# Kernel optimization log

Hardware: AMD Instinct MI355X
Metric: run time of the kernel (lower is better)

The kernel has to match this reference:

```python
import jax, jax.numpy as jnp
import numpy as np
from functools import partial

V, H, B, T, L = 32000, 1024, 64, 64, 4
EOS = 2


def setup_inputs() -> dict:
    key = jax.random.key(0)
    ks = jax.random.split(key, 10)
    s = 1.0 / np.sqrt(H)
    return {
        "max_len": T,
        "tgt": jax.random.randint(ks[0], (B, T), 0, V),
        "h0": jax.random.normal(ks[1], (L, B, H), jnp.float32),
        "c0": jax.random.normal(ks[2], (L, B, H), jnp.float32),
        "embedding": jax.random.normal(ks[3], (V, H), jnp.float32) * s,
        "W_ih": jax.random.normal(ks[4], (L, 4 * H, H), jnp.float32) * s,
        "W_hh": jax.random.normal(ks[5], (L, 4 * H, H), jnp.float32) * s,
        "b_ih": jax.random.normal(ks[6], (L, 4 * H), jnp.float32) * s,
        "b_hh": jax.random.normal(ks[7], (L, 4 * H), jnp.float32) * s,
        "W_cls": jax.random.normal(ks[8], (V, H), jnp.float32) * s,
        "b_cls": jax.random.normal(ks[9], (V,), jnp.float32) * s,
    }


def _lstm_cell(x, h, c, Wi, Wh, bi, bh):
    # gates: [B, 4H] in torch order (i, f, g, o)
    g = x @ Wi.T + bi + h @ Wh.T + bh
    i, f, gg, o = jnp.split(g, 4, axis=-1)
    c2 = jax.nn.sigmoid(f) * c + jax.nn.sigmoid(i) * jnp.tanh(gg)
    h2 = jax.nn.sigmoid(o) * jnp.tanh(c2)
    return h2, c2


def reference(max_len, tgt, h0, c0, embedding, W_ih, W_hh, b_ih, b_hh, W_cls, b_cls):
    # step i>0 uses embedding of tgt[:, i-1].
    batch = tgt.shape[0]
    x0 = jnp.broadcast_to(embedding[EOS], (batch, embedding.shape[1]))
    tf_in = embedding[tgt[:, : max_len - 1]]              # [B, T-1, H]
    inputs = jnp.concatenate([x0[:, None, :], tf_in], axis=1)  # [B, T, H]
    inputs = jnp.swapaxes(inputs, 0, 1)                   # [T, B, H]

    def step(carry, x):
        h, c = carry  # each [L, B, H]
        hs, cs = [], []
        inp = x
        for l in range(L):  # 4 stacked LSTM cells, h of cell l feeds cell l+1
            hn, cn = _lstm_cell(inp, h[l], c[l], W_ih[l], W_hh[l], b_ih[l], b_hh[l])
            hs.append(hn)
            cs.append(cn)
            inp = hn
        h = jnp.stack(hs)
        c = jnp.stack(cs)
        logp = jax.nn.log_softmax(h[L - 1] @ W_cls.T + b_cls, axis=-1)  # [B, V]
        return (h, c), logp

    (h, c), out = jax.lax.scan(step, (h0, c0), inputs)
    return out, h, c  # out: [T, B, V]
```

## Files before the change

### kernel.cpp

```cpp
#include <hip/hip_runtime.h>

using u16 = unsigned short;
using u32 = unsigned int;

typedef __bf16 bf16x8 __attribute__((ext_vector_type(8)));
typedef float  f32x4  __attribute__((ext_vector_type(4)));
typedef u16    u16x8  __attribute__((ext_vector_type(8)));

static constexpr int kV = 32000, kH = 1024, kB = 64, kT = 64, kL = 4, kEOS = 2;

struct Flag { int v; int pad[15]; };

__device__ __forceinline__ u16 f2bf(float f) {
  u32 u = __float_as_uint(f);
  u = (u + 0x7fffu + ((u >> 16) & 1u)) >> 16;
  return (u16)u;
}
__device__ __forceinline__ float sigf(float x)   { return 1.0f / (1.0f + __expf(-x)); }
__device__ __forceinline__ float tanhf_(float x) { return 1.0f - 2.0f / (__expf(2.0f * x) + 1.0f); }

typedef const __attribute__((address_space(1))) u32* gas_ptr;
typedef __attribute__((address_space(3))) u32*       las_ptr;
__device__ __forceinline__ void async16(const u16* g, u16* l) {
  __builtin_amdgcn_global_load_lds((gas_ptr)g, (las_ptr)l, 16, 0, 0);
}

__device__ __forceinline__ void spin_ge(const int* p, int tgt) {
  while (__hip_atomic_load(p, __ATOMIC_RELAXED, __HIP_MEMORY_SCOPE_AGENT) < tgt)
    __builtin_amdgcn_s_sleep(2);
}

__device__ __forceinline__ size_t packed_off(int b, int k) {
  return (size_t)(((b >> 4) * 32 + (k >> 5)) * 512 + (((k >> 3) & 3) * 16 + (b & 15)) * 8 + (k & 7));
}


__global__ void pack_lstm(const float* __restrict__ Wih, const float* __restrict__ Whh,
                          u16* __restrict__ wpack) {
  const int cid  = blockIdx.x * 256 + threadIdx.x;
  const int lane = cid & 63;
  const int cf   = (cid >> 6) & 3;
  const int kk   = (cid >> 8) & 31;
  const int mt   = (cid >> 13) & 1;
  const int blk  = cid >> 14;
  const int lay = blk >> 6, cb = blk & 63;
  const int wr = cf * 1024 + cb * 16 + (lane & 15);
  const int kb = kk * 32 + (lane >> 4) * 8;
  const float* src = (mt ? Whh : Wih) + ((size_t)lay * 4096 + wr) * 1024 + kb;
  const float4* s4 = (const float4*)src;
  float4 v0 = s4[0], v1 = s4[1];
  u16x8 r;
  r[0]=f2bf(v0.x); r[1]=f2bf(v0.y); r[2]=f2bf(v0.z); r[3]=f2bf(v0.w);
  r[4]=f2bf(v1.x); r[5]=f2bf(v1.y); r[6]=f2bf(v1.z); r[7]=f2bf(v1.w);
  *(u16x8*)(wpack + (size_t)cid * 8) = r;
}

__global__ void pack_cls(const float* __restrict__ W, u16* __restrict__ o) {
  const size_t cid = (size_t)blockIdx.x * 256 + threadIdx.x;
  const float4* s4 = (const float4*)(W + cid * 8);
  float4 v0 = s4[0], v1 = s4[1];
  u16x8 r;
  r[0]=f2bf(v0.x); r[1]=f2bf(v0.y); r[2]=f2bf(v0.z); r[3]=f2bf(v0.w);
  r[4]=f2bf(v1.x); r[5]=f2bf(v1.y); r[6]=f2bf(v1.z); r[7]=f2bf(v1.w);
  *(u16x8*)(o + cid * 8) = r;
}

__global__ void pack_x(const float* __restrict__ emb, const int* __restrict__ tgt,
                       u16* __restrict__ X) {
  const int cid = blockIdx.x * 256 + threadIdx.x;
  const int kc = cid & 127, b = (cid >> 7) & 63, t = cid >> 13;
  const int tok = (t == 0) ? kEOS : tgt[b * 64 + t - 1];
  const float4* s4 = (const float4*)(emb + (size_t)tok * 1024 + kc * 8);
  float4 v0 = s4[0], v1 = s4[1];
  u16x8 r;
  r[0]=f2bf(v0.x); r[1]=f2bf(v0.y); r[2]=f2bf(v0.z); r[3]=f2bf(v0.w);
  r[4]=f2bf(v1.x); r[5]=f2bf(v1.y); r[6]=f2bf(v1.z); r[7]=f2bf(v1.w);
  *(u16x8*)(X + (size_t)t * 65536 + packed_off(b, kc * 8)) = r;
}

__global__ void pack_init(const float* __restrict__ h0, const float* __restrict__ bih,
                          const float* __restrict__ bhh, u16* __restrict__ hball,
                          float* __restrict__ bsum) {
  const int cid = blockIdx.x * 256 + threadIdx.x;
  if (cid < 32768) {
    const int kc = cid & 127, row = cid >> 7;
    const int lay = row >> 6, b = row & 63;
    const float4* s4 = (const float4*)(h0 + (size_t)cid * 8);
    float4 v0 = s4[0], v1 = s4[1];
    u16x8 r;
    r[0]=f2bf(v0.x); r[1]=f2bf(v0.y); r[2]=f2bf(v0.z); r[3]=f2bf(v0.w);
    r[4]=f2bf(v1.x); r[5]=f2bf(v1.y); r[6]=f2bf(v1.z); r[7]=f2bf(v1.w);
    *(u16x8*)(hball + (size_t)lay * 65 * 65536 + packed_off(b, kc * 8)) = r;
  } else {
    const int i = cid - 32768;
    bsum[i] = bih[i] + bhh[i];
  }
}

__global__ void __launch_bounds__(1024, 4)
lstm_coop(const u16* __restrict__ wpack, const u16* __restrict__ xall,
          u16* __restrict__ hball, const float* __restrict__ bsum,
          const float* __restrict__ c0, float* __restrict__ outh, float* __restrict__ outc,
          Flag* flags) {
  __shared__ u16 stg[3][32][512];
  __shared__ float Gc[2][64][80];

  const int tid = threadIdx.x, lane = tid & 63, wave = tid >> 6;
  const int l15 = lane & 15, l4 = lane >> 4;
  const int cmat = wave >> 3, cwc = (wave >> 1) & 3, ckh = wave & 1;
  const int blk = blockIdx.x;
  const int lay = (blk >> 1) & 3;
  const int cb  = ((blk >> 3) << 1) | (blk & 1);
  const int u0 = cb << 4;
  const int ub = tid >> 4, uu = tid & 15;

  float creg = c0[((size_t)lay * 64 + ub) * 1024 + u0 + uu];
  float bsv[4];
  #pragma unroll
  for (int g = 0; g < 4; ++g) bsv[g] = bsum[lay * 4096 + g * 1024 + u0 + uu];

  const size_t wbase = (size_t)(lay * 64 + cb) * 131072;
  bf16x8 breg[16];
  #pragma unroll
  for (int j = 0; j < 16; ++j)
    breg[j] = *(const bf16x8*)(wpack + wbase
        + (size_t)(((cmat * 32 + 2 * j + ckh) * 4) + cwc) * 512 + lane * 8);

  const int j0 = wave * 2, j1 = wave * 2 + 1;
  const int m2a = j0 >> 4, mta = (j0 >> 2) & 3, ksla = j0 & 3;
  const int m2b = j1 >> 4, mtb = (j1 >> 2) & 3, kslb = j1 & 3;

  u16* hlay = hball + (size_t)lay * 65 * 65536;
  const u16* hprev = (lay == 0) ? xall : (hball + (size_t)(lay - 1) * 65 * 65536);

  #pragma unroll 1
  for (int t = 0; t < kT; ++t) {
    if (t > 0 && tid < 64)                 spin_ge(&flags[lay * 64 + tid].v, t);
    if (lay > 0 && tid >= 64 && tid < 128) spin_ge(&flags[(lay - 1) * 64 + (tid - 64)].v, t + 1);
    __syncthreads();

    const u16* xsrc = (lay == 0) ? (xall + (size_t)t * 65536)
                                 : (hprev + (size_t)(t + 1) * 65536);
    const u16* hsrc = hlay + (size_t)t * 65536;

    const u16* ga = (m2a ? hsrc : xsrc) + (size_t)((mta * 32 + ksla) * 512) + lane * 8;
    const u16* gb = (m2b ? hsrc : xsrc) + (size_t)((mtb * 32 + kslb) * 512) + lane * 8;

    auto STAGE = [&](int c) {
      async16(ga + (size_t)c * 2048, &stg[c % 3][m2a * 16 + mta * 4 + ksla][0]);
      async16(gb + (size_t)c * 2048, &stg[c % 3][m2b * 16 + mtb * 4 + kslb][0]);
    };

    f32x4 acc[4] = {};
    STAGE(0); STAGE(1);
    #pragma unroll
    for (int c = 0; c < 8; ++c) {
      if (c < 7) asm volatile("s_waitcnt vmcnt(2)" ::: "memory");
      else       asm volatile("s_waitcnt vmcnt(0)" ::: "memory");
      __builtin_amdgcn_s_barrier();
      asm volatile("" ::: "memory");
      if (c < 6) STAGE(c + 2);
      const u16* As = &stg[c % 3][cmat * 16][0];
      #pragma unroll
      for (int s = 0; s < 2; ++s) {
        const int ksl = 2 * s + ckh;
        bf16x8 a[4];
        #pragma unroll
        for (int m = 0; m < 4; ++m)
          a[m] = *(const bf16x8*)(As + (m * 4 + ksl) * 512 + lane * 8);
        #pragma unroll
        for (int m = 0; m < 4; ++m)
          acc[m] = __builtin_amdgcn_mfma_f32_16x16x32_bf16(a[m], breg[2 * c + s], acc[m], 0, 0, 0);
      }
    }

    if (ckh == 0) {
      #pragma unroll
      for (int m = 0; m < 4; ++m)
        #pragma unroll
        for (int r = 0; r < 4; ++r)
          Gc[cmat][m * 16 + l4 * 4 + r][cwc * 16 + l15] = acc[m][r];
    }
    __syncthreads();
    if (ckh == 1) {
      #pragma unroll
      for (int m = 0; m < 4; ++m)
        #pragma unroll
        for (int r = 0; r < 4; ++r)
          Gc[cmat][m * 16 + l4 * 4 + r][cwc * 16 + l15] += acc[m][r];
    }
    __syncthreads();

    float sg[4];
    #pragma unroll
    for (int g = 0; g < 4; ++g) {
      const int col = g * 16 + uu;
      sg[g] = Gc[0][ub][col] + Gc[1][ub][col] + bsv[g];
    }
    const float c2 = sigf(sg[1]) * creg + sigf(sg[0]) * tanhf_(sg[2]);
    const float h2 = sigf(sg[3]) * tanhf_(c2);
    creg = c2;
    const u16 hv = f2bf(h2);
    if (t == kT - 1) {
      outh[((size_t)lay * 64 + ub) * 1024 + u0 + uu] = h2;
      outc[((size_t)lay * 64 + ub) * 1024 + u0 + uu] = c2;
    }
    const u32 other = __shfl_xor((u32)hv, 1);
    if ((tid & 1) == 0) {
      const u32 hpair = (u32)hv | (other << 16);
      u32* hdst = (u32*)(hlay + (size_t)(t + 1) * 65536 + packed_off(ub, u0 + uu));
      __hip_atomic_store(hdst, hpair, __ATOMIC_RELAXED, __HIP_MEMORY_SCOPE_AGENT);
    }
    __syncthreads();
    if (tid == 0)
      __hip_atomic_store(&flags[lay * 64 + cb].v, t + 1, __ATOMIC_RELAXED, __HIP_MEMORY_SCOPE_AGENT);
  }
}

#define CLS_EPILOGUE()                                                                     \
  {                                                                                        \
    float* sR = (float*)&sA[0][0];                                                         \
    _Pragma("unroll")                                                                      \
    for (int mi = 0; mi < 4; ++mi) {                                                       \
      _Pragma("unroll")                                                                    \
      for (int r = 0; r < 4; ++r) {                                                        \
        float v[4];                                                                        \
        _Pragma("unroll")                                                                  \
        for (int ci = 0; ci < 4; ++ci) v[ci] = acc[mi][ci][r] + bc[ci];                     \
        float mx = fmaxf(fmaxf(v[0], v[1]), fmaxf(v[2], v[3]));                            \
        mx = fmaxf(mx, __shfl_xor(mx, 1)); mx = fmaxf(mx, __shfl_xor(mx, 2));              \
        mx = fmaxf(mx, __shfl_xor(mx, 4)); mx = fmaxf(mx, __shfl_xor(mx, 8));              \
        float ss = __expf(v[0]-mx) + __expf(v[1]-mx) + __expf(v[2]-mx) + __expf(v[3]-mx);  \
        ss += __shfl_xor(ss, 1); ss += __shfl_xor(ss, 2);                                  \
        ss += __shfl_xor(ss, 4); ss += __shfl_xor(ss, 8);                                  \
        const int lr = wm * 64 + mi * 16 + l4 * 4 + r;                                     \
        if (wc == 0 && l15 == 0) { sR[lr * 2] = mx; sR[lr * 2 + 1] = ss; }                 \
        __syncthreads();                                                                   \
        if (wc == 1 && l15 == 0) {                                                         \
          const float m0 = sR[lr * 2], s0 = sR[lr * 2 + 1];                                \
          const float M = fmaxf(m0, mx);                                                   \
          const float S = s0 * __expf(m0 - M) + ss * __expf(mx - M);                       \
          const int grow = bm * 128 + lr;                                                  \
          pmax[(size_t)grow * 256 + bn] = M;                                               \
          psum[(size_t)grow * 256 + bn] = S;                                               \
        }                                                                                  \
        __syncthreads();                                                                   \
      }                                                                                    \
    }                                                                                      \
  }

__global__ void __launch_bounds__(256)
cls_gemm(const u16* __restrict__ A, const u16* __restrict__ Bw,
         const float* __restrict__ bcls, float* __restrict__ out,
         float* __restrict__ pmax, float* __restrict__ psum) {
  __shared__ u16 sA[2][4096], sB[2][4096];
  const int tid = threadIdx.x, lane = tid & 63, wave = tid >> 6;
  const int wm = wave >> 1, wc = wave & 1;
  const int l15 = lane & 15, l4 = lane >> 4;
  const int bm = blockIdx.x, bn = blockIdx.y;
  const u16* Ab = A  + (size_t)bm * 131072;
  const u16* Bb = Bw + (size_t)bn * 131072;

  auto STAGE = [&](int kk) {
    u16* dA = sA[kk & 1]; u16* dB = sB[kk & 1];
    #pragma unroll
    for (int q = 0; q < 4; ++q) {
      const int u = wave * 4 + q;
      if (u < 8) {
        const u16* g = Ab + (size_t)(u >> 2) * 65536 + (size_t)(((u & 3) * 32 + kk) * 512) + lane * 8;
        async16(g, dA + u * 512);
      } else {
        const int v = u & 7;
        const u16* g = Bb + (size_t)((v & 1) * 64 + lane) * 1024 + kk * 32 + (v >> 1) * 8;
        async16(g, dB + v * 512);
      }
    }
  };

  f32x4 acc[4][4] = {};
  STAGE(0);
  for (int kk = 0; kk < 32; ++kk) {
    if (kk < 31) { STAGE(kk + 1); asm volatile("s_waitcnt vmcnt(4)" ::: "memory"); }
    else         asm volatile("s_waitcnt vmcnt(0)" ::: "memory");
    __builtin_amdgcn_s_barrier();
    asm volatile("" ::: "memory");
    const u16* aS = sA[kk & 1]; const u16* bS = sB[kk & 1];
    bf16x8 av[4], bv[4];
    #pragma unroll
    for (int mi = 0; mi < 4; ++mi) av[mi] = *(const bf16x8*)(aS + (wm * 4 + mi) * 512 + lane * 8);
    #pragma unroll
    for (int ci = 0; ci < 4; ++ci) bv[ci] = *(const bf16x8*)(bS + l4 * 1024 + (wc * 64 + ci * 16 + l15) * 8);
    #pragma unroll
    for (int mi = 0; mi < 4; ++mi)
      #pragma unroll
      for (int ci = 0; ci < 4; ++ci)
        acc[mi][ci] = __builtin_amdgcn_mfma_f32_16x16x32_bf16(av[mi], bv[ci], acc[mi][ci], 0, 0, 0);
    asm volatile("" ::: "memory");
    __builtin_amdgcn_s_barrier();
  }
  float bc[4];
  #pragma unroll
  for (int ci = 0; ci < 4; ++ci) bc[ci] = bcls[bn * 128 + wc * 64 + ci * 16 + l15];
  #pragma unroll
  for (int ci = 0; ci < 4; ++ci) {
    const int col = bn * 128 + wc * 64 + ci * 16 + l15;
    #pragma unroll
    for (int mi = 0; mi < 4; ++mi)
      #pragma unroll
      for (int r = 0; r < 4; ++r) {
        const int row = bm * 128 + wm * 64 + mi * 16 + l4 * 4 + r;
        out[(size_t)row * 32000 + col] = acc[mi][ci][r] + bc[ci];
      }
  }
  __syncthreads();
  CLS_EPILOGUE()
}

__global__ void __launch_bounds__(256)
cls_gemm_f32(const u16* __restrict__ A, const float* __restrict__ Bw,
             const float* __restrict__ bcls, float* __restrict__ out,
             float* __restrict__ pmax, float* __restrict__ psum) {
  __shared__ u16 sA[2][4096], sB[2][4096];
  const int tid = threadIdx.x, lane = tid & 63, wave = tid >> 6;
  const int wm = wave >> 1, wc = wave & 1;
  const int l15 = lane & 15, l4 = lane >> 4;
  const int bm = blockIdx.x, bn = blockIdx.y;
  const u16*  Ab = A  + (size_t)bm * 131072;
  const float* Bb = Bw + (size_t)bn * 131072;

  auto LOADB = [&](int kk, u16x8* rb) {
    #pragma unroll
    for (int q = 0; q < 2; ++q) {
      const int p = tid + q * 256, row = p & 127, khi = p >> 7;
      const float4* s4 = (const float4*)(Bb + (size_t)row * 1024 + kk * 32 + khi * 8);
      float4 v0 = s4[0], v1 = s4[1];
      u16x8 r;
      r[0]=f2bf(v0.x); r[1]=f2bf(v0.y); r[2]=f2bf(v0.z); r[3]=f2bf(v0.w);
      r[4]=f2bf(v1.x); r[5]=f2bf(v1.y); r[6]=f2bf(v1.z); r[7]=f2bf(v1.w);
      rb[q] = r;
    }
  };
  auto WRITEB = [&](int kk, const u16x8* rb) {
    u16* dB = sB[kk & 1];
    #pragma unroll
    for (int q = 0; q < 2; ++q) *(u16x8*)(dB + (tid + q * 256) * 8) = rb[q];
  };
  auto STAGE_A = [&](int kk) {
    u16* dA = sA[kk & 1];
    #pragma unroll
    for (int q = 0; q < 2; ++q) {
      const int v = wave * 2 + q;
      const u16* g = Ab + (size_t)(v >> 2) * 65536 + (size_t)(((v & 3) * 32 + kk) * 512) + lane * 8;
      async16(g, dA + v * 512);
    }
  };

  f32x4 acc[4][4] = {};
  {
    u16x8 rb[2];
    LOADB(0, rb); STAGE_A(0); WRITEB(0, rb);
  }
  for (int kk = 0; kk < 32; ++kk) {
    if (kk < 31) {
      u16x8 rb[2];
      LOADB(kk + 1, rb);
      STAGE_A(kk + 1);
      WRITEB(kk + 1, rb);
    } else {
      asm volatile("s_waitcnt vmcnt(0)" ::: "memory");
    }
    __builtin_amdgcn_s_barrier();
    asm volatile("" ::: "memory");
    const u16* aS = sA[kk & 1]; const u16* bS = sB[kk & 1];
    bf16x8 av[4], bv[4];
    #pragma unroll
    for (int mi = 0; mi < 4; ++mi) av[mi] = *(const bf16x8*)(aS + (wm * 4 + mi) * 512 + lane * 8);
    #pragma unroll
    for (int ci = 0; ci < 4; ++ci) bv[ci] = *(const bf16x8*)(bS + l4 * 1024 + (wc * 64 + ci * 16 + l15) * 8);
    #pragma unroll
    for (int mi = 0; mi < 4; ++mi)
      #pragma unroll
      for (int ci = 0; ci < 4; ++ci)
        acc[mi][ci] = __builtin_amdgcn_mfma_f32_16x16x32_bf16(av[mi], bv[ci], acc[mi][ci], 0, 0, 0);
    asm volatile("" ::: "memory");
    __builtin_amdgcn_s_barrier();
  }
  float bc[4];
  #pragma unroll
  for (int ci = 0; ci < 4; ++ci) bc[ci] = bcls[bn * 128 + wc * 64 + ci * 16 + l15];
  #pragma unroll
  for (int ci = 0; ci < 4; ++ci) {
    const int col = bn * 128 + wc * 64 + ci * 16 + l15;
    #pragma unroll
    for (int mi = 0; mi < 4; ++mi)
      #pragma unroll
      for (int r = 0; r < 4; ++r) {
        const int row = bm * 128 + wm * 64 + mi * 16 + l4 * 4 + r;
        out[(size_t)row * 32000 + col] = acc[mi][ci][r] + bc[ci];
      }
  }
  __syncthreads();
  CLS_EPILOGUE()
}

__global__ void __launch_bounds__(256)
lsm_red(const float* __restrict__ pmax, const float* __restrict__ psum,
        float* __restrict__ logz) {
  __shared__ float rm[256], rs[256];
  const int r = blockIdx.x, b = threadIdx.x;
  float m = -3.0e38f, s = 0.0f;
  if (b < 250) { m = pmax[(size_t)r * 256 + b]; s = psum[(size_t)r * 256 + b]; }
  rm[b] = m; rs[b] = s; __syncthreads();
  for (int st = 128; st > 0; st >>= 1) {
    if (b < st) {
      const float m2 = rm[b + st], s2 = rs[b + st];
      const float M = fmaxf(rm[b], m2);
      rs[b] = rs[b] * __expf(rm[b] - M) + s2 * __expf(m2 - M);
      rm[b] = M;
    }
    __syncthreads();
  }
  if (b == 0) logz[r] = rm[0] + logf(rs[0]);
}

__global__ void __launch_bounds__(256)
sub_k(float* __restrict__ out, const float* __restrict__ logz) {
  const int r = blockIdx.x;
  const float z = logz[r];
  float4* p = (float4*)(out + (size_t)r * 32000);
  for (int v = threadIdx.x; v < 8000; v += 256) {
    float4 x = p[v];
    x.x -= z; x.y -= z; x.z -= z; x.w -= z;
    p[v] = x;
  }
}

extern "C" void kernel_launch(void* const* d_in, const int* in_sizes, int n_in,
                              void* d_out, int out_size, void* d_ws, size_t ws_size,
                              hipStream_t stream) {
  (void)in_sizes; (void)n_in; (void)out_size;
  const int*   tgt  = (const int*)d_in[1];
  const float* h0   = (const float*)d_in[2];
  const float* c0   = (const float*)d_in[3];
  const float* emb  = (const float*)d_in[4];
  const float* Wih  = (const float*)d_in[5];
  const float* Whh  = (const float*)d_in[6];
  const float* bih  = (const float*)d_in[7];
  const float* bhh  = (const float*)d_in[8];
  const float* Wcls = (const float*)d_in[9];
  const float* bcls = (const float*)d_in[10];

  float* out  = (float*)d_out;
  float* outh = out + (size_t)kT * kB * kV;
  float* outc = outh + (size_t)kL * kB * kH;

  const size_t SZ_WPACK = 67108864;
  const size_t SZ_WCLS  = 65536000;
  const size_t SZ_X     = 8388608;
  const size_t SZ_HBALL = 34078720;
  const size_t SZ_BSUM  = 65536;
  const size_t SZ_FLAGS = 16384;
  const size_t SZ_PM    = 4194304;
  const size_t FULL_REQ = SZ_WPACK + SZ_WCLS + SZ_X + SZ_HBALL + SZ_BSUM + SZ_FLAGS + 2 * SZ_PM + 16384;
  const bool full = (ws_size >= FULL_REQ);

  char* ws = (char*)d_ws;
  size_t off = 0;
  u16* wpack = (u16*)(ws + off); off += SZ_WPACK;
  u16* wclsb = nullptr;
  if (full) { wclsb = (u16*)(ws + off); off += SZ_WCLS; }
  u16*   X     = (u16*)(ws + off); off += SZ_X;
  u16*   hball = (u16*)(ws + off); off += SZ_HBALL;
  float* bsum  = (float*)(ws + off); off += SZ_BSUM;
  Flag*  flags = (Flag*)(ws + off);  off += SZ_FLAGS;
  float* pmax  = (float*)(ws + off); off += SZ_PM;
  float* psum  = (float*)(ws + off); off += SZ_PM;
  float* logz  = (float*)(ws + off); off += 16384;

  pack_lstm<<<16384, 256, 0, stream>>>(Wih, Whh, wpack);
  if (full) pack_cls<<<16000, 256, 0, stream>>>(Wcls, wclsb);
  pack_x   <<<2048,  256, 0, stream>>>(emb, tgt, X);
  pack_init<<<192,   256, 0, stream>>>(h0, bih, bhh, hball, bsum);
  hipMemsetAsync(flags, 0, SZ_FLAGS, stream);

  void* args[] = { (void*)&wpack, (void*)&X, (void*)&hball, (void*)&bsum,
                   (void*)&c0, (void*)&outh, (void*)&outc, (void*)&flags };
  hipLaunchCooperativeKernel((const void*)lstm_coop, dim3(256), dim3(1024), args, 0, stream);

  const u16* h3a = hball + (size_t)3 * 65 * 65536 + 65536;
  if (full) cls_gemm    <<<dim3(32, 250), 256, 0, stream>>>(h3a, wclsb, bcls, out, pmax, psum);
  else      cls_gemm_f32<<<dim3(32, 250), 256, 0, stream>>>(h3a, Wcls,  bcls, out, pmax, psum);
  lsm_red<<<4096, 256, 0, stream>>>(pmax, psum, logz);
  sub_k  <<<4096, 256, 0, stream>>>(out, logz);
}
```

Before: 1.375 ms.

## Pre-tile classifier weights for contiguous async loads and batch softmax epilogue sync

The packed bf16 classifier weights are reordered into per-tile, per-k-step contiguous chunks so each async global-to-LDS load reads a contiguous 1 KB run instead of strided rows. The fp32-weight variant writes its LDS B tile in the same layout. The classifier epilogue now stores both column-halves' row max and sum to shared memory and merges them once after a single barrier, instead of two barriers per row group. This relies on pack_cls, STAGE and WRITEB all agreeing on the new layout.

```diff
diff --git a/kernel.cpp b/kernel.cpp
--- a/kernel.cpp
+++ b/kernel.cpp
@@ -56,13 +56,20 @@
 }
 
 __global__ void pack_cls(const float* __restrict__ W, u16* __restrict__ o) {
-  const size_t cid = (size_t)blockIdx.x * 256 + threadIdx.x;
-  const float4* s4 = (const float4*)(W + cid * 8);
+  const int cid = blockIdx.x * 256 + threadIdx.x;
+  const int bn  = cid >> 14;
+  const int rem = cid & 16383;
+  const int kk  = rem >> 9;
+  const int p   = rem & 511;
+  const int l4  = p >> 7;
+  const int row = p & 127;
+  const float* src = W + ((size_t)(bn * 128 + row)) * 1024 + kk * 32 + l4 * 8;
+  const float4* s4 = (const float4*)src;
   float4 v0 = s4[0], v1 = s4[1];
   u16x8 r;
   r[0]=f2bf(v0.x); r[1]=f2bf(v0.y); r[2]=f2bf(v0.z); r[3]=f2bf(v0.w);
   r[4]=f2bf(v1.x); r[5]=f2bf(v1.y); r[6]=f2bf(v1.z); r[7]=f2bf(v1.w);
-  *(u16x8*)(o + cid * 8) = r;
+  *(u16x8*)(o + (size_t)cid * 8) = r;
 }
 
 __global__ void pack_x(const float* __restrict__ emb, const int* __restrict__ tgt,
@@ -219,7 +226,8 @@
 
 #define CLS_EPILOGUE()                                                                     \
   {                                                                                        \
-    float* sR = (float*)&sA[0][0];                                                         \
+    float* sRm = (float*)&sA[0][0];                                          \
+    float* sRs = sRm + 256;                                                                \
     _Pragma("unroll")                                                                      \
     for (int mi = 0; mi < 4; ++mi) {                                                       \
       _Pragma("unroll")                                                                    \
@@ -234,18 +242,17 @@
         ss += __shfl_xor(ss, 1); ss += __shfl_xor(ss, 2);                                  \
         ss += __shfl_xor(ss, 4); ss += __shfl_xor(ss, 8);                                  \
         const int lr = wm * 64 + mi * 16 + l4 * 4 + r;                                     \
-        if (wc == 0 && l15 == 0) { sR[lr * 2] = mx; sR[lr * 2 + 1] = ss; }                 \
-        __syncthreads();                                                                   \
-        if (wc == 1 && l15 == 0) {                                                         \
-          const float m0 = sR[lr * 2], s0 = sR[lr * 2 + 1];                                \
-          const float M = fmaxf(m0, mx);                                                   \
-          const float S = s0 * __expf(m0 - M) + ss * __expf(mx - M);                       \
-          const int grow = bm * 128 + lr;                                                  \
-          pmax[(size_t)grow * 256 + bn] = M;                                               \
-          psum[(size_t)grow * 256 + bn] = S;                                               \
-        }                                                                                  \
-        __syncthreads();                                                                   \
+        if (l15 == 0) { sRm[wc * 128 + lr] = mx; sRs[wc * 128 + lr] = ss; }                \
       }                                                                                    \
+    }                                                                                      \
+    __syncthreads();                                                                       \
+    if (tid < 128) {                                                                       \
+      const float m0 = sRm[tid], s0 = sRs[tid];                                            \
+      const float m1 = sRm[128 + tid], s1 = sRs[128 + tid];                                \
+      const float M = fmaxf(m0, m1);                                                       \
+      const float S = s0 * __expf(m0 - M) + s1 * __expf(m1 - M);                           \
+      pmax[(size_t)(bm * 128 + tid) * 256 + bn] = M;                                       \
+      psum[(size_t)(bm * 128 + tid) * 256 + bn] = S;                                       \
     }                                                                                      \
   }
 
@@ -271,7 +278,7 @@
         async16(g, dA + u * 512);
       } else {
         const int v = u & 7;
-        const u16* g = Bb + (size_t)((v & 1) * 64 + lane) * 1024 + kk * 32 + (v >> 1) * 8;
+        const u16* g = Bb + (size_t)kk * 4096 + v * 512 + lane * 8;
         async16(g, dB + v * 512);
       }
     }
@@ -343,7 +350,10 @@
   auto WRITEB = [&](int kk, const u16x8* rb) {
     u16* dB = sB[kk & 1];
     #pragma unroll
-    for (int q = 0; q < 2; ++q) *(u16x8*)(dB + (tid + q * 256) * 8) = rb[q];
+    for (int q = 0; q < 2; ++q) {
+      const int p = tid + q * 256, row = p & 127, khi = p >> 7;
+      *(u16x8*)(dB + khi * 1024 + row * 8) = rb[q];
+    }
   };
   auto STAGE_A = [&](int kk) {
     u16* dA = sA[kk & 1];
```

New measurement: 1.329 ms. 3.4% less time.
